# Kernel optimization log

Hardware: AMD Instinct MI355X
Metric: run time of the kernel (lower is better)

The kernel has to match this reference:

```python
import jax, jax.numpy as jnp
import numpy as np

POOL = 7
IMG_H, IMG_W = 1024, 1024
EPS = 1e-3  # keras BatchNormalization default epsilon


def crop_and_resize(fmap, boxes, ph, pw):
    # TF tf.image.crop_and_resize (bilinear), box_indices == batch index of each roi.
    # fmap: [B,H,W,C], boxes: [B,N,4] normalized (y1,x1,y2,x2) -> [B,N,ph,pw,C]
    B, H, W, C = fmap.shape
    y1, x1, y2, x2 = jnp.split(boxes, 4, axis=-1)  # each [B,N,1]
    fy = jnp.arange(ph, dtype=boxes.dtype) / (ph - 1)
    fx = jnp.arange(pw, dtype=boxes.dtype) / (pw - 1)
    ys = (y1 + (y2 - y1) * fy) * (H - 1)  # [B,N,ph]
    xs = (x1 + (x2 - x1) * fx) * (W - 1)  # [B,N,pw]
    y0 = jnp.floor(ys)
    x0 = jnp.floor(xs)
    wy = (ys - y0)[:, :, :, None, None]  # [B,N,ph,1,1]
    wx = (xs - x0)[:, :, None, :, None]  # [B,N,1,pw,1]
    y0i = jnp.clip(y0.astype(jnp.int32), 0, H - 1)
    y1i = jnp.clip(y0i + 1, 0, H - 1)
    x0i = jnp.clip(x0.astype(jnp.int32), 0, W - 1)
    x1i = jnp.clip(x0i + 1, 0, W - 1)
    b = jnp.arange(B)[:, None, None, None]
    yi0 = y0i[:, :, :, None]; yi1 = y1i[:, :, :, None]   # [B,N,ph,1]
    xi0 = x0i[:, :, None, :]; xi1 = x1i[:, :, None, :]   # [B,N,1,pw]
    v00 = fmap[b, yi0, xi0]  # [B,N,ph,pw,C]
    v01 = fmap[b, yi0, xi1]
    v10 = fmap[b, yi1, xi0]
    v11 = fmap[b, yi1, xi1]
    top = v00 + (v01 - v00) * wx
    bot = v10 + (v11 - v10) * wx
    return top + (bot - top) * wy


def pyramid_roi_align(rois, fmaps, pool):
    # rois are stop-gradient in the original layer
    rois = jax.lax.stop_gradient(rois)
    y1, x1, y2, x2 = jnp.split(rois, 4, axis=-1)
    h = y2 - y1
    w = x2 - x1
    scale = 256.0 / np.sqrt(float(IMG_H * IMG_W))
    lvl = jnp.log2(jnp.maximum(jnp.sqrt(h * w), 1e-9) / scale)
    lvl = jnp.clip(4 + jnp.round(lvl).astype(jnp.int32), 2, 5)[..., 0]  # [B,N]
    B, N = rois.shape[:2]
    C = fmaps[0].shape[-1]
    out = jnp.zeros((B, N, pool, pool, C), fmaps[0].dtype)
    for i, fm in enumerate(fmaps):  # levels 2..5, fixed small loop
        sel = (lvl == i + 2)[:, :, None, None, None]
        out = jnp.where(sel, crop_and_resize(fm, rois, pool, pool), out)
    return out


def bn_train(x, gamma, beta):
    # keras BatchNorm with training=True: biased batch stats over all axes but channel
    m = x.mean(axis=(0, 1))
    v = x.var(axis=(0, 1))
    return (x - m) * jax.lax.rsqrt(v + EPS) * gamma + beta


def setup_inputs() -> dict:
    key = jax.random.key(0)
    ks = jax.random.split(key, 12)
    B, N, C, F = 2, 1000, 256, 1024
    # rois: valid boxes, sizes spanning all pyramid levels
    tl = jax.random.uniform(ks[0], (B, N, 2), jnp.float32, 0.0, 0.6)
    sz = jax.random.uniform(ks[1], (B, N, 2), jnp.float32, 0.02, 0.4)
    br = jnp.minimum(tl + sz, 1.0)
    rois = jnp.concatenate([tl[..., :1], tl[..., 1:], br[..., :1], br[..., 1:]], axis=-1)
    s = 0.02
    return {
        "rois": rois,
        "p2": jax.random.normal(ks[2], (B, 256, 256, C), jnp.float32),
        "p3": jax.random.normal(ks[3], (B, 128, 128, C), jnp.float32),
        "p4": jax.random.normal(ks[4], (B, 64, 64, C), jnp.float32),
        "p5": jax.random.normal(ks[5], (B, 32, 32, C), jnp.float32),
        "conv1_w": jax.random.normal(ks[6], (POOL, POOL, C, F), jnp.float32) * s,
        "conv1_b": jnp.zeros((F,), jnp.float32),
        "bn1_g": jnp.ones((F,), jnp.float32),
        "bn1_b": jnp.zeros((F,), jnp.float32),
        "conv2_w": jax.random.normal(ks[7], (F, F), jnp.float32) * s,
        "conv2_b": jnp.zeros((F,), jnp.float32),
        "bn2_g": jnp.ones((F,), jnp.float32),
        "bn2_b": jnp.zeros((F,), jnp.float32),
        "cls_w": jax.random.normal(ks[8], (F, 2), jnp.float32) * s,
        "cls_b": jnp.zeros((2,), jnp.float32),
        "delta_w": jax.random.normal(ks[9], (F, 8), jnp.float32) * s,
        "delta_b": jnp.zeros((8,), jnp.float32),
    }


def reference(rois, p2, p3, p4, p5, conv1_w, conv1_b, bn1_g, bn1_b,
              conv2_w, conv2_b, bn2_g, bn2_b, cls_w, cls_b, delta_w, delta_b):
    B, N = rois.shape[:2]
    n_classes = cls_w.shape[-1]
    pooled = pyramid_roi_align(rois, (p2, p3, p4, p5), POOL)  # [B,N,7,7,C]
    # Conv2D(F,(7,7),'valid') on a 7x7 input == full contraction over (h,w,c)
    x = jnp.einsum('bnhwc,hwcf->bnf', pooled, conv1_w) + conv1_b
    x = jax.nn.relu(bn_train(x, bn1_g, bn1_b))
    x = x @ conv2_w + conv2_b  # 1x1 conv == dense
    shared = jax.nn.relu(bn_train(x, bn2_g, bn2_b))  # [B,N,F]
    logits = shared @ cls_w + cls_b                  # [B,N,n_classes]
    probs = jax.nn.softmax(logits, axis=-1)
    deltas = (shared @ delta_w + delta_b).reshape(B, N, n_classes, 4)
    return logits, probs, deltas
```

## Files before the change

### kernel.cpp

```cpp
#include <hip/hip_runtime.h>
#include <hip/hip_bf16.h>

#define NB     2
#define NROI   1000
#define CIN    256
#define FDIM   1024
#define M_ROWS 2000
#define K1     12544
#define EPSBN  1e-3f
#define MN     (M_ROWS * FDIM)

typedef short bf16x8 __attribute__((ext_vector_type(8)));
typedef short bf16x4 __attribute__((ext_vector_type(4)));
typedef float f32x4  __attribute__((ext_vector_type(4)));

__device__ __forceinline__ void gld_lds16(const void* g, void* l) {
  __builtin_amdgcn_global_load_lds((const __attribute__((address_space(1))) char*)g,
                                   (__attribute__((address_space(3))) char*)l, 16, 0, 0);
}

__global__ __launch_bounds__(256) void prep_kernel(
    const float* __restrict__ rois,
    const float* __restrict__ p2, const float* __restrict__ p3,
    const float* __restrict__ p4, const float* __restrict__ p5,
    __hip_bfloat16* __restrict__ pooled,
    const float* __restrict__ conv1_w, __hip_bfloat16* __restrict__ w1t,
    const float* __restrict__ conv2_w, __hip_bfloat16* __restrict__ w2t,
    float* __restrict__ stats) {
  __shared__ float tt[64][65];
  int idx = blockIdx.x;
  int t = threadIdx.x;

  if (idx == 0) {
#pragma unroll
    for (int i = 0; i < 4; i++)
      ((f32x4*)stats)[t + i * 256] = f32x4{0, 0, 0, 0};
    return;
  }

  if (idx < 1 + M_ROWS) {
    int rn = idx - 1;
    int b = rn / NROI;

    const float* roi = rois + (size_t)rn * 4;
    float y1 = roi[0], x1 = roi[1], y2 = roi[2], x2 = roi[3];
    float h = y2 - y1, w = x2 - x1;
    float lvl = log2f(fmaxf(sqrtf(h * w), 1e-9f) * 4.0f);
    int li = 4 + (int)rintf(lvl);
    li = min(max(li, 2), 5) - 2;

    const float* fm; int H;
    switch (li) {
      case 0:  fm = p2; H = 256; break;
      case 1:  fm = p3; H = 128; break;
      case 2:  fm = p4; H = 64;  break;
      default: fm = p5; H = 32;  break;
    }
    int W = H;
    const float* fb = fm + (size_t)b * H * W * CIN;

    int lane = t & 63, wv = t >> 6;
    int c4 = lane * 4;

    for (int pos = wv; pos < 49; pos += 4) {
      int py = pos / 7, px = pos - py * 7;
      float fy = (float)py / 6.0f, fx = (float)px / 6.0f;
      float ys = (y1 + (y2 - y1) * fy) * (float)(H - 1);
      float xs = (x1 + (x2 - x1) * fx) * (float)(W - 1);
      float y0f = floorf(ys), x0f = floorf(xs);
      float wy = ys - y0f, wx = xs - x0f;
      int y0 = min(max((int)y0f, 0), H - 1);
      int x0 = min(max((int)x0f, 0), W - 1);
      int y1i = min(y0 + 1, H - 1);
      int x1i = min(x0 + 1, W - 1);

      f32x4 v00 = *(const f32x4*)(fb + ((size_t)y0 * W + x0) * CIN + c4);
      f32x4 v01 = *(const f32x4*)(fb + ((size_t)y0 * W + x1i) * CIN + c4);
      f32x4 v10 = *(const f32x4*)(fb + ((size_t)y1i * W + x0) * CIN + c4);
      f32x4 v11 = *(const f32x4*)(fb + ((size_t)y1i * W + x1i) * CIN + c4);

      f32x4 top = v00 + (v01 - v00) * wx;
      f32x4 bot = v10 + (v11 - v10) * wx;
      f32x4 val = top + (bot - top) * wy;

      bf16x4 o;
#pragma unroll
      for (int j = 0; j < 4; j++) {
        __hip_bfloat16 hh = __float2bfloat16(val[j]);
        o[j] = *reinterpret_cast<short*>(&hh);
      }
      *(bf16x4*)((short*)pooled + ((size_t)rn * 49 + pos) * CIN + c4) = o;
    }
    return;
  }

  const float* W; short* WT; int K, N, bx, by;
  if (idx < 1 + M_ROWS + 3136) {
    int wk = idx - (1 + M_ROWS);
    W = conv1_w; WT = (short*)w1t; K = K1; N = FDIM;
    bx = wk % 196; by = wk / 196;
  } else {
    int wk = idx - (1 + M_ROWS + 3136);
    W = conv2_w; WT = (short*)w2t; K = FDIM; N = FDIM;
    bx = wk % 16; by = wk / 16;
  }
  int k0 = bx * 64, n0 = by * 64;
  int r = t >> 2, c = t & 3;
#pragma unroll
  for (int i = 0; i < 4; i++) {
    int cg = c * 4 + i;
    f32x4 v = *(const f32x4*)(W + (size_t)(k0 + r) * N + n0 + cg * 4);
#pragma unroll
    for (int j = 0; j < 4; j++) tt[cg * 4 + j][r] = v[j];
  }
  __syncthreads();
  int n = t >> 2, g = t & 3;
#pragma unroll
  for (int i = 0; i < 2; i++) {
    int seg = g * 2 + i;
    bf16x8 o;
#pragma unroll
    for (int j = 0; j < 8; j++) {
      __hip_bfloat16 hh = __float2bfloat16(tt[n][seg * 8 + j]);
      o[j] = *reinterpret_cast<short*>(&hh);
    }
    *(bf16x8*)(WT + (size_t)(n0 + n) * K + k0 + seg * 8) = o;
  }
}

template<int KSLICES>
__global__ __launch_bounds__(512) void gemm8w(const short* __restrict__ A,
                                              const short* __restrict__ BT,
                                              float* __restrict__ P,
                                              int M, int N, int K) {
  __shared__ short As[4 * 128 * 32];
  __shared__ short Bs[4 * 256 * 32];

  int nwg = gridDim.x;
  int bid = blockIdx.x;
  int cpx = nwg >> 3;
  int wg = (bid & 7) * cpx + (bid >> 3);

  int MT = (M + 127) >> 7;
  int NTn = N >> 8;
  int tiles = MT * NTn;
  int ks = wg / tiles;
  int rem = wg % tiles;
  int tm = rem % MT, tn = rem / MT;
  int m0 = tm * 128, n0 = tn * 256;
  int Kc = K / KSLICES;
  int NT = Kc >> 6;
  size_t kb = (size_t)ks * Kc;

  int tid = threadIdx.x;
  int lane = tid & 63, wid = tid >> 6;
  int wr = wid >> 2, wc = wid & 3;

  int srow = tid >> 2;
  int g = (tid & 3) ^ (srow & 3);
  const short* Agb  = A  + (size_t)min(m0 + srow, M - 1) * K + kb + g * 8;
  const short* Bgb0 = BT + (size_t)(n0 + srow) * K + kb + g * 8;
  const short* Bgb1 = Bgb0 + (size_t)128 * K;
  int aoff  = wid * 512;
  int boff0 = wid * 512;
  int boff1 = 4096 + wid * 512;

  int lr = lane & 15;
  int slotoff = ((lane >> 4) ^ (lane & 3)) * 8;
  const short* Ard = As + (wr * 64 + lr) * 32 + slotoff;
  const short* Brd = Bs + (wc * 64 + lr) * 32 + slotoff;

  f32x4 acc[4][4] = {};

#define STAGE(s) do {                                                        \
    int ts_ = (s) >> 1, kh_ = (s) & 1, b_ = ts_ & 1;                         \
    int ko_ = ts_ * 64 + kh_ * 32;                                           \
    short* Ad_ = (short*)As + (b_ * 2 + kh_) * 4096 + aoff;                  \
    short* Bd_ = (short*)Bs + (b_ * 2 + kh_) * 8192;                         \
    gld_lds16(Agb + ko_, Ad_);                                               \
    gld_lds16(Bgb0 + ko_, Bd_ + boff0);                                      \
    gld_lds16(Bgb1 + ko_, Bd_ + boff1);                                      \
  } while (0)

  STAGE(0); STAGE(1); STAGE(2);

  for (int t = 0; t < NT; ++t) {
    int b = t & 1;
#pragma unroll
    for (int kh = 0; kh < 2; ++kh) {
      __builtin_amdgcn_sched_barrier(0);
      if (t < NT - 1)      asm volatile("s_waitcnt vmcnt(6)" ::: "memory");
      else if (kh == 0)    asm volatile("s_waitcnt vmcnt(3)" ::: "memory");
      else                 asm volatile("s_waitcnt vmcnt(0)" ::: "memory");
      __builtin_amdgcn_s_barrier();
      __builtin_amdgcn_sched_barrier(0);

      const short* Ab = Ard + (b * 2 + kh) * 4096;
      const short* Bb = Brd + (b * 2 + kh) * 8192;
      bf16x8 af[4], bf_[4];
#pragma unroll
      for (int mi = 0; mi < 4; mi++) af[mi] = *(const bf16x8*)(Ab + mi * 512);
#pragma unroll
      for (int ni = 0; ni < 4; ni++) bf_[ni] = *(const bf16x8*)(Bb + ni * 512);

      if (kh == 0) { if (t + 1 < NT) STAGE(2 * t + 3); }
      else         { if (t + 2 < NT) STAGE(2 * t + 4); }

      __builtin_amdgcn_sched_barrier(0);
      asm volatile("s_waitcnt lgkmcnt(0)" ::: "memory");
      __builtin_amdgcn_sched_barrier(0);
      __builtin_amdgcn_s_setprio(1);
#pragma unroll
      for (int mi = 0; mi < 4; mi++)
#pragma unroll
        for (int ni = 0; ni < 4; ni++)
          acc[mi][ni] = __builtin_amdgcn_mfma_f32_16x16x32_bf16(af[mi], bf_[ni], acc[mi][ni], 0, 0, 0);
      __builtin_amdgcn_s_setprio(0);
    }
  }
#undef STAGE

  float* Pb = P + (size_t)ks * M * N;
  int crow = (lane >> 4) * 4, ccol = lane & 15;
#pragma unroll
  for (int mi = 0; mi < 4; mi++) {
    int rb = m0 + wr * 64 + mi * 16 + crow;
#pragma unroll
    for (int ni = 0; ni < 4; ni++) {
      int col = n0 + wc * 64 + ni * 16 + ccol;
#pragma unroll
      for (int r = 0; r < 4; r++) {
        int row = rb + r;
        if (row < M) Pb[(size_t)row * N + col] = acc[mi][ni][r];
      }
    }
  }
}

template<int KS>
__global__ void reduce_bias_stats(const float* __restrict__ P, const float* __restrict__ bias,
                                  float* __restrict__ X, float* __restrict__ stats, int M) {
  int t = threadIdx.x;
  int col = t * 4;
  f32x4 bv = *(const f32x4*)(bias + col);
  f32x4 s = {0, 0, 0, 0}, q = {0, 0, 0, 0};
  for (int r = blockIdx.x; r < M; r += gridDim.x) {
    size_t base = (size_t)r * FDIM + col;
    f32x4 vs[KS];
#pragma unroll
    for (int c = 0; c < KS; c++)
      vs[c] = *(const f32x4*)(P + (size_t)c * MN + base);
    f32x4 v = bv;
#pragma unroll
    for (int c = 0; c < KS; c++) v = v + vs[c];
    *(f32x4*)(X + base) = v;
    s = s + v;
    q = q + v * v;
  }
#pragma unroll
  for (int j = 0; j < 4; j++) {
    atomicAdd(&stats[col + j], s[j]);
    atomicAdd(&stats[FDIM + col + j], q[j]);
  }
}

__global__ void bn_norm_relu_bf16(const float* __restrict__ X, const float* __restrict__ stats,
                                  const float* __restrict__ g, const float* __restrict__ bta,
                                  __hip_bfloat16* __restrict__ obf, int M) {
  int i4 = blockIdx.x * blockDim.x + threadIdx.x;
  if (i4 * 4 >= M * FDIM) return;
  int f = (i4 * 4) & (FDIM - 1);
  f32x4 x  = *(const f32x4*)(X + (size_t)i4 * 4);
  f32x4 sm = *(const f32x4*)(stats + f);
  f32x4 sq = *(const f32x4*)(stats + FDIM + f);
  f32x4 gv = *(const f32x4*)(g + f);
  f32x4 bv = *(const f32x4*)(bta + f);
  float inv_m = 1.0f / (float)M;
  bf16x4 o;
#pragma unroll
  for (int j = 0; j < 4; j++) {
    float mean = sm[j] * inv_m;
    float var = sq[j] * inv_m - mean * mean;
    float xn = (x[j] - mean) * rsqrtf(var + EPSBN) * gv[j] + bv[j];
    __hip_bfloat16 hh = __float2bfloat16(fmaxf(xn, 0.0f));
    o[j] = *reinterpret_cast<short*>(&hh);
  }
  *(bf16x4*)((short*)obf + (size_t)i4 * 4) = o;
}

__global__ void heads_bn(const float* __restrict__ X2, const float* __restrict__ stats,
                         const float* __restrict__ gg, const float* __restrict__ bb,
                         const float* __restrict__ cls_w, const float* __restrict__ cls_b,
                         const float* __restrict__ dw, const float* __restrict__ db,
                         float* __restrict__ out) {
  int row = blockIdx.x * 4 + (threadIdx.x >> 6);
  int lane = threadIdx.x & 63;
  if (row >= M_ROWS) return;
  const float* xrow = X2 + (size_t)row * FDIM;
  float inv_m = 1.0f / (float)M_ROWS;
  float a[10];
#pragma unroll
  for (int j = 0; j < 10; j++) a[j] = 0.0f;
  for (int k = lane; k < FDIM; k += 64) {
    float mean = stats[k] * inv_m;
    float var = stats[FDIM + k] * inv_m - mean * mean;
    float v = fmaxf((xrow[k] - mean) * rsqrtf(var + EPSBN) * gg[k] + bb[k], 0.0f);
    a[0] += v * cls_w[k * 2 + 0];
    a[1] += v * cls_w[k * 2 + 1];
#pragma unroll
    for (int j = 0; j < 8; j++) a[2 + j] += v * dw[k * 8 + j];
  }
#pragma unroll
  for (int j = 0; j < 10; j++)
    for (int o = 32; o > 0; o >>= 1) a[j] += __shfl_xor(a[j], o, 64);
  if (lane == 0) {
    float l0 = a[0] + cls_b[0], l1 = a[1] + cls_b[1];
    out[row * 2 + 0] = l0;
    out[row * 2 + 1] = l1;
    float mx = fmaxf(l0, l1);
    float e0 = expf(l0 - mx), e1 = expf(l1 - mx);
    float inv = 1.0f / (e0 + e1);
    out[4000 + row * 2 + 0] = e0 * inv;
    out[4000 + row * 2 + 1] = e1 * inv;
#pragma unroll
    for (int j = 0; j < 8; j++) out[8000 + row * 8 + j] = a[2 + j] + db[j];
  }
}

extern "C" void kernel_launch(void* const* d_in, const int* in_sizes, int n_in,
                              void* d_out, int out_size, void* d_ws, size_t ws_size,
                              hipStream_t stream) {
  const float* rois    = (const float*)d_in[0];
  const float* p2      = (const float*)d_in[1];
  const float* p3      = (const float*)d_in[2];
  const float* p4      = (const float*)d_in[3];
  const float* p5      = (const float*)d_in[4];
  const float* conv1_w = (const float*)d_in[5];
  const float* conv1_b = (const float*)d_in[6];
  const float* bn1_g   = (const float*)d_in[7];
  const float* bn1_b   = (const float*)d_in[8];
  const float* conv2_w = (const float*)d_in[9];
  const float* conv2_b = (const float*)d_in[10];
  const float* bn2_g   = (const float*)d_in[11];
  const float* bn2_b   = (const float*)d_in[12];
  const float* cls_w   = (const float*)d_in[13];
  const float* cls_b   = (const float*)d_in[14];
  const float* delta_w = (const float*)d_in[15];
  const float* delta_b = (const float*)d_in[16];
  float* out = (float*)d_out;

  char* ws = (char*)d_ws;
  size_t off = 0;
  __hip_bfloat16* pooled = (__hip_bfloat16*)(ws + off); off += (size_t)M_ROWS * K1 * 2;
  __hip_bfloat16* w1t    = (__hip_bfloat16*)(ws + off); off += (size_t)K1 * FDIM * 2;
  __hip_bfloat16* w2t    = (__hip_bfloat16*)(ws + off); off += (size_t)FDIM * FDIM * 2;
  float* stats1          = (float*)(ws + off);          off += 2 * FDIM * 4;
  float* stats2          = (float*)(ws + off);          off += 2 * FDIM * 4;
  char*  Preg            = ws + off;                    off += (size_t)4 * MN * 4;
  float* part1        = (float*)Preg;
  float* x1           = (float*)Preg;
  __hip_bfloat16* x1n = (__hip_bfloat16*)pooled;
  float* part2        = (float*)Preg;
  float* x2           = (float*)Preg;

  prep_kernel<<<1 + M_ROWS + 3136 + 256, 256, 0, stream>>>(
      rois, p2, p3, p4, p5, pooled, conv1_w, w1t, conv2_w, w2t, stats1);

  gemm8w<4><<<256, 512, 0, stream>>>((const short*)pooled, (const short*)w1t, part1,
                                     M_ROWS, FDIM, K1);
  reduce_bias_stats<4><<<256, 256, 0, stream>>>(part1, conv1_b, x1, stats1, M_ROWS);

  bn_norm_relu_bf16<<<MN / 1024, 256, 0, stream>>>(x1, stats1, bn1_g, bn1_b, x1n, M_ROWS);

  gemm8w<4><<<256, 512, 0, stream>>>((const short*)x1n, (const short*)w2t, part2,
                                     M_ROWS, FDIM, FDIM);
  reduce_bias_stats<4><<<256, 256, 0, stream>>>(part2, conv2_b, x2, stats2, M_ROWS);

  heads_bn<<<(M_ROWS + 3) / 4, 256, 0, stream>>>(x2, stats2, bn2_g, bn2_b,
                                                 cls_w, cls_b, delta_w, delta_b, out);

  (void)in_sizes; (void)n_in; (void)out_size; (void)ws_size;
}
```

Baseline: 206.1 us.

## Fuse split-K reduction with BN apply and heads via grid-wide barrier

Merges the split-K reduce/statistics kernel with the BN-normalize kernel, and the second reduce with the heads kernel, using a software grid barrier built on an atomic counter (zeroed in prep, stored right after the stats buffers). After the barrier each block computes per-channel scale and shift into LDS, and the heads weights are transposed into LDS. This removes two kernel launches and an extra pass over the fp32 activations, since rows are reread by the block that wrote them. The risk is deadlock if all 256 blocks are not co-resident, plus a small serial barrier cost.

```diff
diff --git a/kernel.cpp b/kernel.cpp
--- a/kernel.cpp
+++ b/kernel.cpp
@@ -17,6 +17,17 @@
 __device__ __forceinline__ void gld_lds16(const void* g, void* l) {
   __builtin_amdgcn_global_load_lds((const __attribute__((address_space(1))) char*)g,
                                    (__attribute__((address_space(3))) char*)l, 16, 0, 0);
+}
+
+__device__ __forceinline__ void grid_sync(int* cnt, int nb) {
+  __syncthreads();
+  if (threadIdx.x == 0) {
+    __threadfence();
+    atomicAdd(cnt, 1);
+    while (atomicAdd(cnt, 0) < nb) { }
+    __threadfence();
+  }
+  __syncthreads();
 }
 
 __global__ __launch_bounds__(256) void prep_kernel(
@@ -35,6 +46,7 @@
 #pragma unroll
     for (int i = 0; i < 4; i++)
       ((f32x4*)stats)[t + i * 256] = f32x4{0, 0, 0, 0};
+    if (t < 2) ((int*)(stats + 4096))[t] = 0;
     return;
   }
 
@@ -238,13 +250,17 @@
 }
 
 template<int KS>
-__global__ void reduce_bias_stats(const float* __restrict__ P, const float* __restrict__ bias,
-                                  float* __restrict__ X, float* __restrict__ stats, int M) {
-  int t = threadIdx.x;
+__global__ __launch_bounds__(256) void reduce_bn_fused(
+    const float* __restrict__ P, const float* __restrict__ bias,
+    float* __restrict__ X, float* __restrict__ stats, int* __restrict__ cnt,
+    const float* __restrict__ g, const float* __restrict__ bta,
+    __hip_bfloat16* __restrict__ obf, int M) {
+  __shared__ float sscale[FDIM], sshift[FDIM];
+  int t = threadIdx.x, b = blockIdx.x;
   int col = t * 4;
   f32x4 bv = *(const f32x4*)(bias + col);
   f32x4 s = {0, 0, 0, 0}, q = {0, 0, 0, 0};
-  for (int r = blockIdx.x; r < M; r += gridDim.x) {
+  for (int r = b; r < M; r += 256) {
     size_t base = (size_t)r * FDIM + col;
     f32x4 vs[KS];
 #pragma unroll
@@ -262,68 +278,118 @@
     atomicAdd(&stats[col + j], s[j]);
     atomicAdd(&stats[FDIM + col + j], q[j]);
   }
-}
-
-__global__ void bn_norm_relu_bf16(const float* __restrict__ X, const float* __restrict__ stats,
-                                  const float* __restrict__ g, const float* __restrict__ bta,
-                                  __hip_bfloat16* __restrict__ obf, int M) {
-  int i4 = blockIdx.x * blockDim.x + threadIdx.x;
-  if (i4 * 4 >= M * FDIM) return;
-  int f = (i4 * 4) & (FDIM - 1);
-  f32x4 x  = *(const f32x4*)(X + (size_t)i4 * 4);
-  f32x4 sm = *(const f32x4*)(stats + f);
-  f32x4 sq = *(const f32x4*)(stats + FDIM + f);
-  f32x4 gv = *(const f32x4*)(g + f);
-  f32x4 bv = *(const f32x4*)(bta + f);
+
+  grid_sync(cnt, 256);
+
   float inv_m = 1.0f / (float)M;
-  bf16x4 o;
+  for (int i = t; i < FDIM; i += 256) {
+    float sm = atomicAdd(&stats[i], 0.0f);
+    float sq = atomicAdd(&stats[FDIM + i], 0.0f);
+    float mean = sm * inv_m;
+    float var = sq * inv_m - mean * mean;
+    float sc = rsqrtf(var + EPSBN) * g[i];
+    sscale[i] = sc;
+    sshift[i] = bta[i] - mean * sc;
+  }
+  __syncthreads();
+
+  f32x4 scv = *(const f32x4*)(sscale + col);
+  f32x4 shv = *(const f32x4*)(sshift + col);
+  for (int r = b; r < M; r += 256) {
+    size_t base = (size_t)r * FDIM + col;
+    f32x4 x = *(const f32x4*)(X + base);
+    bf16x4 o;
+#pragma unroll
+    for (int j = 0; j < 4; j++) {
+      __hip_bfloat16 hh = __float2bfloat16(fmaxf(x[j] * scv[j] + shv[j], 0.0f));
+      o[j] = *reinterpret_cast<short*>(&hh);
+    }
+    *(bf16x4*)((short*)obf + base) = o;
+  }
+}
+
+template<int KS>
+__global__ __launch_bounds__(256) void reduce_heads_fused(
+    const float* __restrict__ P, const float* __restrict__ bias,
+    float* __restrict__ X, float* __restrict__ stats, int* __restrict__ cnt,
+    const float* __restrict__ gg, const float* __restrict__ bb,
+    const float* __restrict__ cls_w, const float* __restrict__ cls_b,
+    const float* __restrict__ dw, const float* __restrict__ db,
+    float* __restrict__ out, int M) {
+  __shared__ float sscale[FDIM], sshift[FDIM];
+  __shared__ float clsT[2][FDIM];
+  __shared__ float dwT[8][FDIM];
+  int t = threadIdx.x, b = blockIdx.x;
+  int col = t * 4;
+  f32x4 bv = *(const f32x4*)(bias + col);
+  f32x4 s = {0, 0, 0, 0}, q = {0, 0, 0, 0};
+  for (int r = b; r < M; r += 256) {
+    size_t base = (size_t)r * FDIM + col;
+    f32x4 vs[KS];
+#pragma unroll
+    for (int c = 0; c < KS; c++)
+      vs[c] = *(const f32x4*)(P + (size_t)c * MN + base);
+    f32x4 v = bv;
+#pragma unroll
+    for (int c = 0; c < KS; c++) v = v + vs[c];
+    *(f32x4*)(X + base) = v;
+    s = s + v;
+    q = q + v * v;
+  }
 #pragma unroll
   for (int j = 0; j < 4; j++) {
-    float mean = sm[j] * inv_m;
-    float var = sq[j] * inv_m - mean * mean;
-    float xn = (x[j] - mean) * rsqrtf(var + EPSBN) * gv[j] + bv[j];
-    __hip_bfloat16 hh = __float2bfloat16(fmaxf(xn, 0.0f));
-    o[j] = *reinterpret_cast<short*>(&hh);
-  }
-  *(bf16x4*)((short*)obf + (size_t)i4 * 4) = o;
-}
-
-__global__ void heads_bn(const float* __restrict__ X2, const float* __restrict__ stats,
-                         const float* __restrict__ gg, const float* __restrict__ bb,
-                         const float* __restrict__ cls_w, const float* __restrict__ cls_b,
-                         const float* __restrict__ dw, const float* __restrict__ db,
-                         float* __restrict__ out) {
-  int row = blockIdx.x * 4 + (threadIdx.x >> 6);
-  int lane = threadIdx.x & 63;
-  if (row >= M_ROWS) return;
-  const float* xrow = X2 + (size_t)row * FDIM;
-  float inv_m = 1.0f / (float)M_ROWS;
-  float a[10];
-#pragma unroll
-  for (int j = 0; j < 10; j++) a[j] = 0.0f;
-  for (int k = lane; k < FDIM; k += 64) {
-    float mean = stats[k] * inv_m;
-    float var = stats[FDIM + k] * inv_m - mean * mean;
-    float v = fmaxf((xrow[k] - mean) * rsqrtf(var + EPSBN) * gg[k] + bb[k], 0.0f);
-    a[0] += v * cls_w[k * 2 + 0];
-    a[1] += v * cls_w[k * 2 + 1];
-#pragma unroll
-    for (int j = 0; j < 8; j++) a[2 + j] += v * dw[k * 8 + j];
-  }
-#pragma unroll
-  for (int j = 0; j < 10; j++)
-    for (int o = 32; o > 0; o >>= 1) a[j] += __shfl_xor(a[j], o, 64);
-  if (lane == 0) {
-    float l0 = a[0] + cls_b[0], l1 = a[1] + cls_b[1];
-    out[row * 2 + 0] = l0;
-    out[row * 2 + 1] = l1;
-    float mx = fmaxf(l0, l1);
-    float e0 = expf(l0 - mx), e1 = expf(l1 - mx);
-    float inv = 1.0f / (e0 + e1);
-    out[4000 + row * 2 + 0] = e0 * inv;
-    out[4000 + row * 2 + 1] = e1 * inv;
-#pragma unroll
-    for (int j = 0; j < 8; j++) out[8000 + row * 8 + j] = a[2 + j] + db[j];
+    atomicAdd(&stats[col + j], s[j]);
+    atomicAdd(&stats[FDIM + col + j], q[j]);
+  }
+
+  grid_sync(cnt, 256);
+
+  float inv_m = 1.0f / (float)M;
+  for (int i = t; i < FDIM; i += 256) {
+    float sm = atomicAdd(&stats[i], 0.0f);
+    float sq = atomicAdd(&stats[FDIM + i], 0.0f);
+    float mean = sm * inv_m;
+    float var = sq * inv_m - mean * mean;
+    float sc = rsqrtf(var + EPSBN) * gg[i];
+    sscale[i] = sc;
+    sshift[i] = bb[i] - mean * sc;
+    clsT[0][i] = cls_w[i * 2];
+    clsT[1][i] = cls_w[i * 2 + 1];
+#pragma unroll
+    for (int j = 0; j < 8; j++) dwT[j][i] = dw[i * 8 + j];
+  }
+  __syncthreads();
+
+  int lane = t & 63, wv = t >> 6;
+  for (int k = wv; k < 8; k += 4) {
+    int row = b + (k << 8);
+    if (row >= M) break;
+    const float* xrow = X + (size_t)row * FDIM;
+    float a[10];
+#pragma unroll
+    for (int j = 0; j < 10; j++) a[j] = 0.0f;
+    for (int kk = lane; kk < FDIM; kk += 64) {
+      float v = fmaxf(xrow[kk] * sscale[kk] + sshift[kk], 0.0f);
+      a[0] += v * clsT[0][kk];
+      a[1] += v * clsT[1][kk];
+#pragma unroll
+      for (int j = 0; j < 8; j++) a[2 + j] += v * dwT[j][kk];
+    }
+#pragma unroll
+    for (int j = 0; j < 10; j++)
+      for (int o = 32; o > 0; o >>= 1) a[j] += __shfl_xor(a[j], o, 64);
+    if (lane == 0) {
+      float l0 = a[0] + cls_b[0], l1 = a[1] + cls_b[1];
+      out[row * 2 + 0] = l0;
+      out[row * 2 + 1] = l1;
+      float mx = fmaxf(l0, l1);
+      float e0 = expf(l0 - mx), e1 = expf(l1 - mx);
+      float inv = 1.0f / (e0 + e1);
+      out[4000 + row * 2 + 0] = e0 * inv;
+      out[4000 + row * 2 + 1] = e1 * inv;
+#pragma unroll
+      for (int j = 0; j < 8; j++) out[8000 + row * 8 + j] = a[2 + j] + db[j];
+    }
   }
 }
 
@@ -356,6 +422,7 @@
   __hip_bfloat16* w2t    = (__hip_bfloat16*)(ws + off); off += (size_t)FDIM * FDIM * 2;
   float* stats1          = (float*)(ws + off);          off += 2 * FDIM * 4;
   float* stats2          = (float*)(ws + off);          off += 2 * FDIM * 4;
+  int*   cnts            = (int*)(ws + off);            off += 256;
   char*  Preg            = ws + off;                    off += (size_t)4 * MN * 4;
   float* part1        = (float*)Preg;
   float* x1           = (float*)Preg;
@@ -368,16 +435,14 @@
 
   gemm8w<4><<<256, 512, 0, stream>>>((const short*)pooled, (const short*)w1t, part1,
                                      M_ROWS, FDIM, K1);
-  reduce_bias_stats<4><<<256, 256, 0, stream>>>(part1, conv1_b, x1, stats1, M_ROWS);
-
-  bn_norm_relu_bf16<<<MN / 1024, 256, 0, stream>>>(x1, stats1, bn1_g, bn1_b, x1n, M_ROWS);
+  reduce_bn_fused<4><<<256, 256, 0, stream>>>(part1, conv1_b, x1, stats1, &cnts[0],
+                                              bn1_g, bn1_b, x1n, M_ROWS);
 
   gemm8w<4><<<256, 512, 0, stream>>>((const short*)x1n, (const short*)w2t, part2,
                                      M_ROWS, FDIM, FDIM);
-  reduce_bias_stats<4><<<256, 256, 0, stream>>>(part2, conv2_b, x2, stats2, M_ROWS);
-
-  heads_bn<<<(M_ROWS + 3) / 4, 256, 0, stream>>>(x2, stats2, bn2_g, bn2_b,
-                                                 cls_w, cls_b, delta_w, delta_b, out);
+  reduce_heads_fused<4><<<256, 256, 0, stream>>>(part2, conv2_b, x2, stats2, &cnts[1],
+                                                 bn2_g, bn2_b, cls_w, cls_b,
+                                                 delta_w, delta_b, out, M_ROWS);
 
   (void)in_sizes; (void)n_in; (void)out_size; (void)ws_size;
 }
```

After: 261.2 us. +26.7%, slower.
